# Kernel tuning notes

Hardware: AMD Instinct MI355X
Metric: run time of the kernel (lower is better)

Reference implementation:

```python
import jax, jax.numpy as jnp
import numpy as np
from jax import lax

B, N, C, H, W = 2, 32, 64, 128, 128
ROI_H = ROI_W = 28
RATIO = 2  # ROIAlign sampling_ratio


def setup_inputs() -> dict:
    key = jax.random.key(0)
    ks = jax.random.split(key, 20)
    p = lambda k, s: jax.random.normal(k, s, jnp.float32) * 0.05
    inp = {}
    inp['cnn_feature'] = jax.random.normal(ks[0], (B, C, H, W), jnp.float32)
    inp['act_ind'] = jax.random.randint(ks[1], (B, N), 0, H * W)
    inp['awh'] = jax.random.uniform(ks[2], (B, N, 2), jnp.float32, minval=4.0, maxval=40.0)
    # fusion: 4 convs (64->256, then 256->256 x3), all 3x3 pad 1
    inp['w1'] = p(ks[3], (256, 64, 3, 3)); inp['b1'] = jnp.zeros((256,), jnp.float32)
    inp['w2'] = p(ks[4], (256, 256, 3, 3)); inp['b2'] = jnp.zeros((256,), jnp.float32)
    inp['w3'] = p(ks[5], (256, 256, 3, 3)); inp['b3'] = jnp.zeros((256,), jnp.float32)
    inp['w4'] = p(ks[6], (256, 256, 3, 3)); inp['b4'] = jnp.zeros((256,), jnp.float32)
    # cp_hm head: deconv(256->256,k2,s2) + conv1x1(256->1), bias -2.19
    inp['hm_dw'] = p(ks[7], (256, 256, 2, 2))  # torch ConvTranspose layout [in,out,kh,kw]
    inp['hm_db'] = jnp.zeros((256,), jnp.float32)
    inp['hm_w'] = p(ks[8], (1, 256, 1, 1)); inp['hm_b'] = jnp.full((1,), -2.19, jnp.float32)
    # cp_wh head: deconv(256->256,k2,s2) + conv1x1(256->2), bias 0
    inp['wh_dw'] = p(ks[9], (256, 256, 2, 2))
    inp['wh_db'] = jnp.zeros((256,), jnp.float32)
    inp['wh_w'] = p(ks[10], (2, 256, 1, 1)); inp['wh_b'] = jnp.zeros((2,), jnp.float32)
    return inp


def conv(x, w, b, pad):
    y = lax.conv_general_dilated(x, w, (1, 1), pad, dimension_numbers=('NCHW', 'OIHW', 'NCHW'))
    return y + b[None, :, None, None]


def deconv2x2s2(x, w, b):
    # matches torch ConvTranspose2d(k=2, s=2, pad=0) with weight [in,out,2,2]
    y = lax.conv_transpose(x, w, (2, 2), 'VALID', dimension_numbers=('NCHW', 'IOHW', 'NCHW'), transpose_kernel=True)
    return y + b[None, :, None, None]


def roi_align(feat, b_idx, boxes):
    # feat [B,C,H,W], boxes [R,4] (x1,y1,x2,y2), spatial_scale=1, sampling_ratio=RATIO
    x1, y1, x2, y2 = boxes[:, 0], boxes[:, 1], boxes[:, 2], boxes[:, 3]
    bw = (x2 - x1) / ROI_W
    bh = (y2 - y1) / ROI_H
    sx = jnp.arange(ROI_W * RATIO)
    sy = jnp.arange(ROI_H * RATIO)
    # sample coord for bin i, sub-sample k: start + (i + (k+0.5)/ratio) * bin
    fx = (sx // RATIO).astype(jnp.float32) + ((sx % RATIO).astype(jnp.float32) + 0.5) / RATIO
    fy = (sy // RATIO).astype(jnp.float32) + ((sy % RATIO).astype(jnp.float32) + 0.5) / RATIO
    xs = x1[:, None] + fx[None, :] * bw[:, None]   # [R,Sx]
    ys = y1[:, None] + fy[None, :] * bh[:, None]   # [R,Sy]

    def sample_one(bi, ysr, xsr):
        img = feat[bi]                              # [C,H,W]
        ysr = jnp.clip(ysr, 0.0, H - 1.0)
        xsr = jnp.clip(xsr, 0.0, W - 1.0)
        y0 = jnp.floor(ysr).astype(jnp.int32); y1i = jnp.minimum(y0 + 1, H - 1); wy = ysr - y0
        x0 = jnp.floor(xsr).astype(jnp.int32); x1i = jnp.minimum(x0 + 1, W - 1); wx = xsr - x0
        # separable bilinear: interpolate rows, then columns
        rows = img[:, y0, :] * (1.0 - wy)[None, :, None] + img[:, y1i, :] * wy[None, :, None]  # [C,Sy,W]
        vals = rows[:, :, x0] * (1.0 - wx)[None, None, :] + rows[:, :, x1i] * wx[None, None, :]  # [C,Sy,Sx]
        # average RATIO x RATIO samples per bin
        v = vals.reshape(C, ROI_H, RATIO, ROI_W, RATIO)
        return v.mean(axis=(2, 4))                  # [C,ROI_H,ROI_W]

    return jax.vmap(sample_one)(b_idx, ys, xs)      # [R,C,ROI_H,ROI_W]


def reference(cnn_feature, act_ind, awh, w1, b1, w2, b2, w3, b3, w4, b4,
              hm_dw, hm_db, hm_w, hm_b, wh_dw, wh_db, wh_w, wh_b):
    # --- prepare_training: decode boxes from act_ind + awh (act_01 all ones) ---
    xs = (act_ind % W).astype(jnp.float32)          # [B,N]
    ys = (act_ind // W).astype(jnp.float32)
    half_w = awh[..., 0] / 2.0
    half_h = awh[..., 1] / 2.0
    boxes = jnp.stack([xs - half_w, ys - half_h, xs + half_w, ys + half_h], axis=-1)  # [B,N,4]
    boxes = boxes.reshape(B * N, 4)
    b_idx = jnp.repeat(jnp.arange(B), N)
    roi = roi_align(cnn_feature, b_idx, boxes)      # [R,64,28,28]
    # --- fusion convs ---
    x = jax.nn.relu(conv(roi, w1, b1, 'SAME'))
    x = jax.nn.relu(conv(x, w2, b2, 'SAME'))
    x = jax.nn.relu(conv(x, w3, b3, 'SAME'))
    x = jax.nn.relu(conv(x, w4, b4, 'SAME'))        # [R,256,28,28]
    # --- heads ---
    cp_hm = conv(deconv2x2s2(x, hm_dw, hm_db), hm_w, hm_b, 'VALID')  # [R,1,56,56]
    cp_wh = conv(deconv2x2s2(x, wh_dw, wh_db), wh_w, wh_b, 'VALID')  # [R,2,56,56]
    return jnp.concatenate([cp_hm, cp_wh], axis=1)  # [R,3,56,56]
```

## Files before the change

kernel.cpp:

```cpp
#include <hip/hip_runtime.h>
#include <hip/hip_bf16.h>

#define HWF 128
#define NB  64
#define PW  30
#define PP  900

using bf16 = __hip_bfloat16;
typedef __attribute__((ext_vector_type(8)))  short short8;
typedef __attribute__((ext_vector_type(4)))  float f32x4;
typedef __attribute__((ext_vector_type(16))) float f32x16;
typedef __attribute__((ext_vector_type(4)))  unsigned int u32x4;
typedef __attribute__((ext_vector_type(2)))  unsigned int u32x2;

__device__ __forceinline__ float b2f(bf16 v) { return __bfloat162float(v); }
__device__ __forceinline__ bf16  f2b(float v){ return __float2bfloat16(v); }
__device__ __forceinline__ float u2f(unsigned short u){ unsigned x = (unsigned)u << 16; float f; __builtin_memcpy(&f,&x,4); return f; }
__device__ __forceinline__ unsigned pack2(float a, float b) {
  union { bf16 h; unsigned short u; } ca, cb; ca.h = f2b(a); cb.h = f2b(b);
  return ((unsigned)cb.u << 16) | (unsigned)ca.u;
}

__global__ void weff_kernel(const float* __restrict__ hm_dw, const float* __restrict__ hm_db,
                            const float* __restrict__ hm_w,  const float* __restrict__ hm_b,
                            const float* __restrict__ wh_dw, const float* __restrict__ wh_db,
                            const float* __restrict__ wh_w,  const float* __restrict__ wh_b,
                            float* __restrict__ Weff, float* __restrict__ beff) {
  const int blk = blockIdx.x;
  const int k = blk / 3, o = blk % 3;
  const int ci = threadIdx.x;
  const float* dw = (o == 0) ? hm_dw : wh_dw;
  const float* hw = (o == 0) ? hm_w  : (wh_w + (size_t)(o - 1) * 256);
  const float* dwp = dw + (size_t)ci * 4 + k;
  float s = 0.f;
  for (int co = 0; co < 256; ++co) s += hw[co] * dwp[(size_t)co * 1024];
  Weff[(size_t)blk * 256 + ci] = s;
  if (k == 0 && ci == 0) {
    const float* db = (o == 0) ? hm_db : wh_db;
    float bb = (o == 0) ? hm_b[0] : wh_b[o - 1];
    float t = 0.f;
    for (int co = 0; co < 256; ++co) t += hw[co] * db[co];
    beff[o] = bb + t;
  }
}

__global__ void wt_kernel(const float* __restrict__ w, bf16* __restrict__ Wt, int CIN) {
  const int co = blockIdx.x, ci = threadIdx.x;
  const int NCIB = CIN >> 5;
  const int cib = ci >> 5, cl = ci & 31;
  const int kh = cl >> 4, koct = (cl >> 3) & 1, e = ci & 7;
  for (int tap = 0; tap < 9; ++tap)
    Wt[(((((size_t)tap * NCIB + cib) * 2 + kh) * 256 + co) * 2 + koct) * 8 + e]
        = f2b(w[((size_t)co * CIN + ci) * 9 + tap]);
}

__global__ __launch_bounds__(256) void featT_kernel(const float* __restrict__ feat,
                                                    bf16* __restrict__ featT) {
  const int by = blockIdx.x;
  const int b = by >> 7, y = by & 127;
  const int t = threadIdx.x;
  __shared__ float tile[128][65];
  const int xr = t & 127, c2 = t >> 7;
  for (int c0 = 0; c0 < 64; c0 += 2)
    tile[xr][c0 + c2] = feat[(((size_t)(b * 64 + c0 + c2) * 128 + y) * 128) + xr];
  __syncthreads();
  const int cw = t & 63, x4 = t >> 6;
  for (int x0 = 0; x0 < 128; x0 += 4)
    featT[(((size_t)by * 128) + x0 + x4) * 64 + cw] = f2b(tile[x0 + x4][cw]);
}

__global__ __launch_bounds__(256) void roi_cl(const bf16* __restrict__ featT,
                                              const int* __restrict__ act_ind,
                                              const float* __restrict__ awh,
                                              bf16* __restrict__ roiP) {
  const int r = blockIdx.x, part = blockIdx.y;
  const int t = threadIdx.x;
  if (part == 7) {
    for (int i = t; i < 116 * 64; i += 256) {
      int j = i >> 6, c = i & 63;
      int py, px;
      if (j < 30)      { py = 0;      px = j;      }
      else if (j < 60) { py = 29;     px = j - 30; }
      else if (j < 88) { py = j - 59; px = 0;      }
      else             { py = j - 87; px = 29;     }
      roiP[(((size_t)(r * 2 + (c >> 5)) * PP) + py * PW + px) * 32 + (c & 31)] = f2b(0.f);
    }
    return;
  }
  const int wave = t >> 6, c = t & 63;
  const int bi = r >> 5;
  const int ind = act_ind[r];
  const float cx = (float)(ind % HWF), cy = (float)(ind / HWF);
  const float hw = awh[r * 2 + 0] * 0.5f, hh = awh[r * 2 + 1] * 0.5f;
  const float x1b = cx - hw, y1b = cy - hh;
  const float bw = hw / 14.f, bh = hh / 14.f;
  const bf16* fb = featT + (size_t)bi * HWF * HWF * 64;
  for (int pp = part * 112 + wave; pp < part * 112 + 112; pp += 4) {
    int ry = pp / 28, rx = pp % 28;
    float acc = 0.f;
#pragma unroll
    for (int a = 0; a < 2; ++a) {
      int syi = 2 * ry + a;
      float ys = y1b + ((float)syi * 0.5f + 0.25f) * bh;
      ys = fminf(fmaxf(ys, 0.f), 127.f);
      int y0 = (int)floorf(ys); int y1i = min(y0 + 1, 127);
      float wy = ys - (float)y0;
#pragma unroll
      for (int b2 = 0; b2 < 2; ++b2) {
        int sxi = 2 * rx + b2;
        float xs = x1b + ((float)sxi * 0.5f + 0.25f) * bw;
        xs = fminf(fmaxf(xs, 0.f), 127.f);
        int x0 = (int)floorf(xs); int x1i = min(x0 + 1, 127);
        float wx = xs - (float)x0;
        float v00 = b2f(fb[((size_t)y0  * HWF + x0 ) * 64 + c]);
        float v01 = b2f(fb[((size_t)y0  * HWF + x1i) * 64 + c]);
        float v10 = b2f(fb[((size_t)y1i * HWF + x0 ) * 64 + c]);
        float v11 = b2f(fb[((size_t)y1i * HWF + x1i) * 64 + c]);
        float r0 = v00 * (1.f - wy) + v10 * wy;
        float r1 = v01 * (1.f - wy) + v11 * wy;
        acc += r0 * (1.f - wx) + r1 * wx;
      }
    }
    int slot = (ry + 1) * PW + (rx + 1);
    roiP[(((size_t)(r * 2 + (c >> 5)) * PP) + slot) * 32 + (c & 31)] = f2b(acc * 0.25f);
  }
}

template <int CIN>
__global__ __launch_bounds__(128, 2) void conv_mfma(const bf16* __restrict__ X,
                                                    const bf16* __restrict__ Wt,
                                                    const float* __restrict__ bias,
                                                    bf16* __restrict__ Y) {
  constexpr int NCIB = CIN / 32;
  const int d = blockIdx.x;
  const int xcd = d & 7, sub = d >> 3;
  const int img = xcd * 8 + (sub >> 4);
  const int sm  = sub & 15;
  const int sb  = sm >> 2;
  const int mg  = sm & 3;
  const int s0  = 30 + sb * 210;
  const int gbase = s0 - 31;
  const int t = threadIdx.x;
  const int wave = t >> 6, lane = t & 63;
  const int hi = lane >> 5, l31 = lane & 31;
  const int ng = wave;

  __shared__ char lds_raw[71680];
  char* Ab = lds_raw;
  char* Bb = lds_raw + 36864;

  int bsrc[9]; bool bok[9];
#pragma unroll
  for (int r = 0; r < 9; ++r) {
    int chunk = r * 128 + t;
    bok[r] = (chunk < 1088);
    int ss = chunk >> 2, up = chunk & 3;
    int u = up ^ ((ss >> 2) & 3);
    int q = gbase + ss; q = q < 0 ? 0 : (q > 899 ? 899 : q);
    bsrc[r] = q * 64 + u * 16;
  }

#define STAGE_B(BSEL, CIB)                                                       \
  {                                                                              \
    const char* Xc = (const char*)X + ((size_t)(img * NCIB + (CIB)) * 900) * 64; \
    _Pragma("unroll")                                                            \
    for (int r = 0; r < 9; ++r) {                                                \
      if (bok[r]) {                                                              \
        __builtin_amdgcn_global_load_lds(                                        \
            (const __attribute__((address_space(1))) unsigned int*)(Xc + bsrc[r]),\
            (__attribute__((address_space(3))) unsigned int*)                    \
                (Bb + (BSEL) * 17408 + (r * 128 + t) * 16), 16, 0, 0);           \
      }                                                                          \
    }                                                                            \
  }

  int asr[9];
#pragma unroll
  for (int r = 0; r < 9; ++r) {
    int chunk = r * 128 + t;
    int tap = chunk >> 7, within = chunk & 127;
    int s = within ^ ((within >> 3) & 7);
    asr[r] = tap * (NCIB * 2 * 8192) + mg * 2048 + s * 16;
  }

#define STAGE_A(CIB, KH, ABSEL)                                                  \
  {                                                                              \
    const char* Wb = (const char*)Wt + ((CIB) * 2 + (KH)) * 8192;                \
    _Pragma("unroll")                                                            \
    for (int r = 0; r < 9; ++r) {                                                \
      __builtin_amdgcn_global_load_lds(                                          \
          (const __attribute__((address_space(1))) unsigned int*)(Wb + asr[r]),  \
          (__attribute__((address_space(3))) unsigned int*)                      \
              (Ab + (ABSEL) * 18432 + (r * 128 + t) * 16), 16, 0, 0);            \
    }                                                                            \
  }

  f32x16 acc[2][4];
#pragma unroll
  for (int mf = 0; mf < 2; ++mf)
#pragma unroll
    for (int nf = 0; nf < 4; ++nf)
#pragma unroll
      for (int e = 0; e < 16; ++e) acc[mf][nf][e] = 0.f;

  int soc[4];
#pragma unroll
  for (int nf = 0; nf < 4; ++nf) {
    int so = ng * 105 + nf * 32 + l31;
    soc[nf] = (so > 209 ? 209 : so) + 31;
  }
  const int gl0 = 2 * l31 + hi;
  const int apos = (gl0 ^ ((gl0 >> 3) & 7)) * 16;

  constexpr int DTP9[9] = { -31, -30, -29, -1, 0, 1, 29, 30, 31 };

#define LOADA(A, AB, T)                                                          \
  {                                                                              \
    _Pragma("unroll")                                                            \
    for (int mf = 0; mf < 2; ++mf)                                               \
      A[mf] = *(const short8*)((AB) + (T) * 2048 + mf * 1024 + apos);            \
  }

#define LOADB(B, LB, T, KH)                                                      \
  {                                                                              \
    _Pragma("unroll")                                                            \
    for (int nf = 0; nf < 4; ++nf) {                                             \
      int ss = soc[nf] + DTP9[(T)];                                              \
      int u = (((KH) << 1) + hi) ^ ((ss >> 2) & 3);                              \
      B[nf] = *(const short8*)((LB) + ss * 64 + (u << 4));                       \
    }                                                                            \
  }

#define DOMFMA(A, B)                                                             \
  {                                                                              \
    _Pragma("unroll")                                                            \
    for (int mf = 0; mf < 2; ++mf)                                               \
      _Pragma("unroll")                                                          \
      for (int nf = 0; nf < 4; ++nf)                                             \
        acc[mf][nf] = __builtin_amdgcn_mfma_f32_32x32x16_bf16(                   \
            A[mf], B[nf], acc[mf][nf], 0, 0, 0);                                 \
  }

#define JLOOP(KH, AB, LB)                                                        \
  {                                                                              \
    short8 a0[2], b0[4], a1[2], b1[4];                                           \
    LOADA(a0, AB, 0); LOADB(b0, LB, 0, KH);                                      \
    LOADA(a1, AB, 1); LOADB(b1, LB, 1, KH);                                      \
    DOMFMA(a0, b0);                                                              \
    LOADA(a0, AB, 2); LOADB(b0, LB, 2, KH);                                      \
    DOMFMA(a1, b1);                                                              \
    LOADA(a1, AB, 3); LOADB(b1, LB, 3, KH);                                      \
    DOMFMA(a0, b0);                                                              \
    LOADA(a0, AB, 4); LOADB(b0, LB, 4, KH);                                      \
    DOMFMA(a1, b1);                                                              \
    LOADA(a1, AB, 5); LOADB(b1, LB, 5, KH);                                      \
    DOMFMA(a0, b0);                                                              \
    LOADA(a0, AB, 6); LOADB(b0, LB, 6, KH);                                      \
    DOMFMA(a1, b1);                                                              \
    LOADA(a1, AB, 7); LOADB(b1, LB, 7, KH);                                      \
    DOMFMA(a0, b0);                                                              \
    LOADA(a0, AB, 8); LOADB(b0, LB, 8, KH);                                      \
    DOMFMA(a1, b1);                                                              \
    DOMFMA(a0, b0);                                                              \
  }

  STAGE_A(0, 0, 0);
  STAGE_B(0, 0);
  __syncthreads();

  int cur = 0;
  for (int cib = 0; cib < NCIB; ++cib) {
    STAGE_A(cib, 1, 1);
    if (cib + 1 < NCIB) STAGE_B(cur ^ 1, cib + 1);
    JLOOP(0, Ab, Bb + cur * 17408);
    __syncthreads();
    if (cib + 1 < NCIB) STAGE_A(cib + 1, 0, 0);
    JLOOP(1, Ab + 18432, Bb + cur * 17408);
    __syncthreads();
    cur ^= 1;
  }

  {
    f32x4 bv[2][4];
#pragma unroll
    for (int mf = 0; mf < 2; ++mf)
#pragma unroll
      for (int rq = 0; rq < 4; ++rq)
        bv[mf][rq] = *(const f32x4*)(bias + mg * 64 + mf * 32 + 8 * rq + 4 * hi);
#pragma unroll
    for (int mf = 0; mf < 2; ++mf) {
#pragma unroll
      for (int nf = 0; nf < 4; ++nf) {
        int so = ng * 105 + nf * 32 + l31;
        if (so < 210) {
#pragma unroll
          for (int rq = 0; rq < 4; ++rq) {
            float r0 = fmaxf(acc[mf][nf][4*rq+0] + bv[mf][rq][0], 0.f);
            float r1 = fmaxf(acc[mf][nf][4*rq+1] + bv[mf][rq][1], 0.f);
            float r2 = fmaxf(acc[mf][nf][4*rq+2] + bv[mf][rq][2], 0.f);
            float r3 = fmaxf(acc[mf][nf][4*rq+3] + bv[mf][rq][3], 0.f);
            u32x2 pk; pk.x = pack2(r0, r1); pk.y = pack2(r2, r3);
            int cb = mf * 64 + rq * 16 + hi * 8;
            *(u32x2*)(lds_raw + so * 128 + ((cb + so * 8) & 127)) = pk;
          }
        }
      }
    }
  }
  __syncthreads();

  {
#pragma unroll
    for (int p = 0; p < 14; ++p) {
      int idx = p * 128 + t;
      if (idx < 1680) {
        int slot = idx >> 3, rem = idx & 7;
        int cob_l = rem >> 2, q = rem & 3;
        int gslot = s0 + slot;
        int c = gslot % 30;
        u32x4 o;
        if (c == 0 || c == 29) { o.x = 0u; o.y = 0u; o.z = 0u; o.w = 0u; }
        else {
          int cb0 = cob_l * 64 + q * 16;
          u32x2 v0 = *(u32x2*)(lds_raw + slot * 128 + ((cb0 + 0 + slot * 8) & 127));
          u32x2 v1 = *(u32x2*)(lds_raw + slot * 128 + ((cb0 + 8 + slot * 8) & 127));
          o.x = v0.x; o.y = v0.y; o.z = v1.x; o.w = v1.y;
        }
        *(u32x4*)((char*)Y + ((size_t)(img * 8 + mg * 2 + cob_l) * 900 + gslot) * 64
                  + q * 16) = o;
      }
    }
  }
  if (sb == 0 || sb == 3) {
    const int rowslot = (sb == 0) ? 0 : 870;
    for (int i = t; i < 240; i += 128) {
      int slot_z = i >> 3, rem = i & 7;
      int cob_l = rem >> 2, q = rem & 3;
      u32x4 z; z.x = 0u; z.y = 0u; z.z = 0u; z.w = 0u;
      *(u32x4*)((char*)Y + ((size_t)(img * 8 + mg * 2 + cob_l) * 900
                + rowslot + slot_z) * 64 + q * 16) = z;
    }
  }
}

__global__ __launch_bounds__(256) void head_cl(const bf16* __restrict__ X,
                                               const float* __restrict__ Weff,
                                               const float* __restrict__ beff,
                                               float* __restrict__ out) {
  const int idx = blockIdx.x * 256 + threadIdx.x;
  const int img = idx / 784, p = idx % 784;
  const float bo0 = beff[0], bo1 = beff[1], bo2 = beff[2];
  int iy = p / 28, ix = p % 28;
  int slot = (iy + 1) * PW + ix + 1;
  float acc[12];
#pragma unroll
  for (int k = 0; k < 12; ++k) acc[k] = 0.f;
  for (int cob = 0; cob < 8; ++cob) {
    const bf16* xp = X + ((size_t)(img * 8 + cob) * PP + slot) * 32;
#pragma unroll
    for (int oct = 0; oct < 4; ++oct) {
      short8 v = *(const short8*)(xp + oct * 8);
#pragma unroll
      for (int j = 0; j < 8; ++j) {
        float xv = u2f((unsigned short)v[j]);
        int ci = cob * 32 + oct * 8 + j;
#pragma unroll
        for (int k = 0; k < 12; ++k)
          acc[k] += xv * Weff[k * 256 + ci];
      }
    }
  }
#pragma unroll
  for (int k4 = 0; k4 < 4; ++k4) {
    int oy = 2 * iy + (k4 >> 1), ox = 2 * ix + (k4 & 1);
    out[(((size_t)(img * 3 + 0)) * 56 + oy) * 56 + ox] = acc[k4 * 3 + 0] + bo0;
    out[(((size_t)(img * 3 + 1)) * 56 + oy) * 56 + ox] = acc[k4 * 3 + 1] + bo1;
    out[(((size_t)(img * 3 + 2)) * 56 + oy) * 56 + ox] = acc[k4 * 3 + 2] + bo2;
  }
}

extern "C" void kernel_launch(void* const* d_in, const int* in_sizes, int n_in,
                              void* d_out, int out_size, void* d_ws, size_t ws_size,
                              hipStream_t stream) {
  const float* feat    = (const float*)d_in[0];
  const int*   act_ind = (const int*)  d_in[1];
  const float* awh     = (const float*)d_in[2];
  const float* w1 = (const float*)d_in[3];  const float* b1 = (const float*)d_in[4];
  const float* w2 = (const float*)d_in[5];  const float* b2 = (const float*)d_in[6];
  const float* w3 = (const float*)d_in[7];  const float* b3 = (const float*)d_in[8];
  const float* w4 = (const float*)d_in[9];  const float* b4 = (const float*)d_in[10];
  const float* hm_dw = (const float*)d_in[11]; const float* hm_db = (const float*)d_in[12];
  const float* hm_w  = (const float*)d_in[13]; const float* hm_b  = (const float*)d_in[14];
  const float* wh_dw = (const float*)d_in[15]; const float* wh_db = (const float*)d_in[16];
  const float* wh_w  = (const float*)d_in[17]; const float* wh_b  = (const float*)d_in[18];

  char* ws = (char*)d_ws;
  size_t offset = 0;
  auto alloc = [&](size_t bytes) {
    size_t r = offset;
    offset += (bytes + 255) & ~(size_t)255;
    return r;
  };
  float* Weff = (float*)(ws + alloc(12 * 256 * sizeof(float)));
  float* beff = (float*)(ws + alloc(256));
  bf16*  Wt1  = (bf16*)(ws + alloc((size_t)9 * 256 * 64  * 2));
  bf16*  Wt2  = (bf16*)(ws + alloc((size_t)9 * 256 * 256 * 2));
  bf16*  Wt3  = (bf16*)(ws + alloc((size_t)9 * 256 * 256 * 2));
  bf16*  Wt4  = (bf16*)(ws + alloc((size_t)9 * 256 * 256 * 2));
  bf16*  bufA = (bf16*)(ws + alloc((size_t)NB * 256 * PP * 2));
  bf16*  bufB = (bf16*)(ws + alloc((size_t)NB * 256 * PP * 2));
  bf16*  roiP  = bufB;
  bf16*  featT = (bf16*)((char*)bufB + (8u << 20));

  weff_kernel<<<12, 256, 0, stream>>>(hm_dw, hm_db, hm_w, hm_b,
                                      wh_dw, wh_db, wh_w, wh_b, Weff, beff);
  wt_kernel<<<256, 64,  0, stream>>>(w1, Wt1, 64);
  wt_kernel<<<256, 256, 0, stream>>>(w2, Wt2, 256);
  wt_kernel<<<256, 256, 0, stream>>>(w3, Wt3, 256);
  wt_kernel<<<256, 256, 0, stream>>>(w4, Wt4, 256);
  featT_kernel<<<256, 256, 0, stream>>>(feat, featT);
  roi_cl<<<dim3(NB, 8), 256, 0, stream>>>(featT, act_ind, awh, roiP);
  conv_mfma<64> <<<1024, 128, 0, stream>>>(roiP, Wt1, b1, bufA);
  conv_mfma<256><<<1024, 128, 0, stream>>>(bufA, Wt2, b2, bufB);
  conv_mfma<256><<<1024, 128, 0, stream>>>(bufB, Wt3, b3, bufA);
  conv_mfma<256><<<1024, 128, 0, stream>>>(bufA, Wt4, b4, bufB);
  head_cl<<<196, 256, 0, stream>>>(bufB, Weff, beff, (float*)d_out);
}
```

Measured before the change: 361.1 us.

## Single-buffer conv staging to cut LDS and fuse weight prep kernels

The conv kernel drops double-buffered activation staging. It now loads both weight halves and the activation block together and then computes, which shrinks LDS so more blocks can be resident per CU. The exchange is losing the overlap of global->LDS copies with MFMA work, since there are now two barriers per channel block with the loads exposed. Separately, the weight-effective and four weight-transpose kernels are merged into one launch to cut launch overhead.

```diff
diff --git a/kernel.cpp b/kernel.cpp
--- a/kernel.cpp
+++ b/kernel.cpp
@@ -21,37 +21,51 @@
   return ((unsigned)cb.u << 16) | (unsigned)ca.u;
 }
 
-__global__ void weff_kernel(const float* __restrict__ hm_dw, const float* __restrict__ hm_db,
-                            const float* __restrict__ hm_w,  const float* __restrict__ hm_b,
-                            const float* __restrict__ wh_dw, const float* __restrict__ wh_db,
-                            const float* __restrict__ wh_w,  const float* __restrict__ wh_b,
-                            float* __restrict__ Weff, float* __restrict__ beff) {
-  const int blk = blockIdx.x;
-  const int k = blk / 3, o = blk % 3;
+__global__ __launch_bounds__(256) void prep_kernel(
+    const float* __restrict__ hm_dw, const float* __restrict__ hm_db,
+    const float* __restrict__ hm_w,  const float* __restrict__ hm_b,
+    const float* __restrict__ wh_dw, const float* __restrict__ wh_db,
+    const float* __restrict__ wh_w,  const float* __restrict__ wh_b,
+    float* __restrict__ Weff, float* __restrict__ beff,
+    const float* __restrict__ w1, bf16* __restrict__ Wt1,
+    const float* __restrict__ w2, bf16* __restrict__ Wt2,
+    const float* __restrict__ w3, bf16* __restrict__ Wt3,
+    const float* __restrict__ w4, bf16* __restrict__ Wt4) {
+  const int b = blockIdx.x;
+  if (b < 12) {
+    const int k = b / 3, o = b % 3;
+    const int ci = threadIdx.x;
+    const float* dw = (o == 0) ? hm_dw : wh_dw;
+    const float* hw = (o == 0) ? hm_w  : (wh_w + (size_t)(o - 1) * 256);
+    const float* dwp = dw + (size_t)ci * 4 + k;
+    float s = 0.f;
+    for (int co = 0; co < 256; ++co) s += hw[co] * dwp[(size_t)co * 1024];
+    Weff[(size_t)b * 256 + ci] = s;
+    if (k == 0 && ci == 0) {
+      const float* db = (o == 0) ? hm_db : wh_db;
+      float bb = (o == 0) ? hm_b[0] : wh_b[o - 1];
+      float t = 0.f;
+      for (int co = 0; co < 256; ++co) t += hw[co] * db[co];
+      beff[o] = bb + t;
+    }
+    return;
+  }
+  const int i = b - 12;
+  const int layer = i >> 8, co = i & 255;
+  const float* w; bf16* Wt; int CIN;
+  if      (layer == 0) { w = w1; Wt = Wt1; CIN = 64;  }
+  else if (layer == 1) { w = w2; Wt = Wt2; CIN = 256; }
+  else if (layer == 2) { w = w3; Wt = Wt3; CIN = 256; }
+  else                 { w = w4; Wt = Wt4; CIN = 256; }
   const int ci = threadIdx.x;
-  const float* dw = (o == 0) ? hm_dw : wh_dw;
-  const float* hw = (o == 0) ? hm_w  : (wh_w + (size_t)(o - 1) * 256);
-  const float* dwp = dw + (size_t)ci * 4 + k;
-  float s = 0.f;
-  for (int co = 0; co < 256; ++co) s += hw[co] * dwp[(size_t)co * 1024];
-  Weff[(size_t)blk * 256 + ci] = s;
-  if (k == 0 && ci == 0) {
-    const float* db = (o == 0) ? hm_db : wh_db;
-    float bb = (o == 0) ? hm_b[0] : wh_b[o - 1];
-    float t = 0.f;
-    for (int co = 0; co < 256; ++co) t += hw[co] * db[co];
-    beff[o] = bb + t;
-  }
-}
-
-__global__ void wt_kernel(const float* __restrict__ w, bf16* __restrict__ Wt, int CIN) {
-  const int co = blockIdx.x, ci = threadIdx.x;
-  const int NCIB = CIN >> 5;
-  const int cib = ci >> 5, cl = ci & 31;
-  const int kh = cl >> 4, koct = (cl >> 3) & 1, e = ci & 7;
-  for (int tap = 0; tap < 9; ++tap)
-    Wt[(((((size_t)tap * NCIB + cib) * 2 + kh) * 256 + co) * 2 + koct) * 8 + e]
-        = f2b(w[((size_t)co * CIN + ci) * 9 + tap]);
+  if (ci < CIN) {
+    const int NCIB = CIN >> 5;
+    const int cib = ci >> 5, cl = ci & 31;
+    const int kh = cl >> 4, koct = (cl >> 3) & 1, e = ci & 7;
+    for (int tap = 0; tap < 9; ++tap)
+      Wt[(((((size_t)tap * NCIB + cib) * 2 + kh) * 256 + co) * 2 + koct) * 8 + e]
+          = f2b(w[((size_t)co * CIN + ci) * 9 + tap]);
+  }
 }
 
 __global__ __launch_bounds__(256) void featT_kernel(const float* __restrict__ feat,
@@ -145,7 +159,7 @@
   const int hi = lane >> 5, l31 = lane & 31;
   const int ng = wave;
 
-  __shared__ char lds_raw[71680];
+  __shared__ char lds_raw[54272];
   char* Ab = lds_raw;
   char* Bb = lds_raw + 36864;
 
@@ -160,7 +174,7 @@
     bsrc[r] = q * 64 + u * 16;
   }
 
-#define STAGE_B(BSEL, CIB)                                                       \
+#define STAGE_B(CIB)                                                             \
   {                                                                              \
     const char* Xc = (const char*)X + ((size_t)(img * NCIB + (CIB)) * 900) * 64; \
     _Pragma("unroll")                                                            \
@@ -169,7 +183,7 @@
         __builtin_amdgcn_global_load_lds(                                        \
             (const __attribute__((address_space(1))) unsigned int*)(Xc + bsrc[r]),\
             (__attribute__((address_space(3))) unsigned int*)                    \
-                (Bb + (BSEL) * 17408 + (r * 128 + t) * 16), 16, 0, 0);           \
+                (Bb + (r * 128 + t) * 16), 16, 0, 0);                            \
       }                                                                          \
     }                                                                            \
   }
@@ -265,19 +279,20 @@
   }
 
   STAGE_A(0, 0, 0);
-  STAGE_B(0, 0);
+  STAGE_A(0, 1, 1);
+  STAGE_B(0);
   __syncthreads();
 
-  int cur = 0;
   for (int cib = 0; cib < NCIB; ++cib) {
-    STAGE_A(cib, 1, 1);
-    if (cib + 1 < NCIB) STAGE_B(cur ^ 1, cib + 1);
-    JLOOP(0, Ab, Bb + cur * 17408);
+    JLOOP(0, Ab, Bb);
+    JLOOP(1, Ab + 18432, Bb);
     __syncthreads();
-    if (cib + 1 < NCIB) STAGE_A(cib + 1, 0, 0);
-    JLOOP(1, Ab + 18432, Bb + cur * 17408);
-    __syncthreads();
-    cur ^= 1;
+    if (cib + 1 < NCIB) {
+      STAGE_A(cib + 1, 0, 0);
+      STAGE_A(cib + 1, 1, 1);
+      STAGE_B(cib + 1);
+      __syncthreads();
+    }
   }
 
   {
@@ -412,12 +427,9 @@
   bf16*  roiP  = bufB;
   bf16*  featT = (bf16*)((char*)bufB + (8u << 20));
 
-  weff_kernel<<<12, 256, 0, stream>>>(hm_dw, hm_db, hm_w, hm_b,
-                                      wh_dw, wh_db, wh_w, wh_b, Weff, beff);
-  wt_kernel<<<256, 64,  0, stream>>>(w1, Wt1, 64);
-  wt_kernel<<<256, 256, 0, stream>>>(w2, Wt2, 256);
-  wt_kernel<<<256, 256, 0, stream>>>(w3, Wt3, 256);
-  wt_kernel<<<256, 256, 0, stream>>>(w4, Wt4, 256);
+  prep_kernel<<<1036, 256, 0, stream>>>(hm_dw, hm_db, hm_w, hm_b,
+                                        wh_dw, wh_db, wh_w, wh_b, Weff, beff,
+                                        w1, Wt1, w2, Wt2, w3, Wt3, w4, Wt4);
   featT_kernel<<<256, 256, 0, stream>>>(feat, featT);
   roi_cl<<<dim3(NB, 8), 256, 0, stream>>>(featT, act_ind, awh, roiP);
   conv_mfma<64> <<<1024, 128, 0, stream>>>(roiP, Wt1, b1, bufA);
```

After: 447.4 us. 1.24x slower.
